# Performance work log

Hardware: AMD Instinct MI355X
Metric: run time of the kernel (lower is better)

## Reference

```python
import jax, jax.numpy as jnp
import numpy as np

EPS = 1e-12  # matches torch F.normalize default eps


def _l2norm(x):
    # F.normalize(x, dim=-1): x / max(||x||, eps)
    n = jnp.sqrt(jnp.sum(x * x, axis=-1, keepdims=True))
    return x / jnp.maximum(n, EPS)


def setup_inputs() -> dict:
    key = jax.random.key(0)
    kq, kk, kv = jax.random.split(key, 3)
    B, H, N, D = 8, 16, 1024, 64
    q = jax.random.normal(kq, (B, H, N, D), dtype=jnp.float32)
    k = jax.random.normal(kk, (B, H, N, D), dtype=jnp.float32)
    v = jax.random.normal(kv, (B, H, N, D), dtype=jnp.float32)
    return {"q": q, "k": k, "v": v}


def reference(q, k, v):
    B, H, N, D = q.shape
    qn = _l2norm(q)  # [B,H,N,D]
    kn = _l2norm(k)  # [B,H,N,D]
    # cosine-similarity attention logits: [B,H,N,N]
    attn = jnp.einsum("bhnd,bhmd->bhnm", qn, kn)
    attn = jax.nn.softmax(attn, axis=-1)
    # attn_drop is identity (p=0)
    x = jnp.einsum("bhnm,bhmd->bhnd", attn, v)  # [B,H,N,D]
    # transpose(1,2).reshape(B, -1, H*D)
    x = jnp.transpose(x, (0, 2, 1, 3)).reshape(B, N, H * D)
    return x
```

## Files before the change

### kernel.cpp

```cpp
#include <hip/hip_runtime.h>
#include <stdint.h>

typedef __attribute__((ext_vector_type(8))) short short8;
typedef __attribute__((ext_vector_type(4))) float floatx4;

#define B_   8
#define H_   16
#define N_   1024
#define D_   64
#define NH_  (B_*H_)
#define LOG2E 1.44269504088896340736f

extern "C" {
__device__ float __ocml_native_exp2_f32(float);
__device__ float __ocml_native_rsqrt_f32(float);
}

__device__ __forceinline__ unsigned int pk2(float a, float b) {
    unsigned int ua = __float_as_uint(a) + 0x8000u;
    unsigned int ub = __float_as_uint(b) + 0x8000u;
    return __builtin_amdgcn_perm(ub, ua, 0x07060302);
}

__global__ __launch_bounds__(256, 2) void attn_fused(
    const float* __restrict__ q, const float* __restrict__ k,
    const float* __restrict__ v, float* __restrict__ out)
{
    __shared__ __align__(16) unsigned short ks[2][64 * 64];
    __shared__ __align__(16) unsigned short vt[2][64 * 64];

    const int bid = blockIdx.x;
    const int xcd = bid & 7, rest = bid >> 3;
    const int qt = rest & 3;
    const int head = (rest >> 2) * 8 + xcd;
    const int tid = threadIdx.x, w = tid >> 6, lane = tid & 63;
    const int lam = lane & 15, quad = lane >> 4;
    const int sw = lam & 7;
    const int q0 = qt * 256 + w * 64;

    const float* qh = q + ((size_t)head * N_ + q0) * D_;
    const float* kh = k + (size_t)head * N_ * D_;
    const float* vh = v + (size_t)head * N_ * D_;

    short8 aq[4][2];
    #pragma unroll
    for (int t = 0; t < 4; t++) {
        const float* qr = qh + (t * 16 + lam) * D_ + quad * 8;
        float4 f0 = *(const float4*)(qr);
        float4 f1 = *(const float4*)(qr + 4);
        float4 f2 = *(const float4*)(qr + 32);
        float4 f3 = *(const float4*)(qr + 36);
        float ss = f0.x*f0.x + f0.y*f0.y + f0.z*f0.z + f0.w*f0.w
                 + f1.x*f1.x + f1.y*f1.y + f1.z*f1.z + f1.w*f1.w
                 + f2.x*f2.x + f2.y*f2.y + f2.z*f2.z + f2.w*f2.w
                 + f3.x*f3.x + f3.y*f3.y + f3.z*f3.z + f3.w*f3.w;
        ss += __shfl_xor(ss, 16);
        ss += __shfl_xor(ss, 32);
        float sc = LOG2E * __ocml_native_rsqrt_f32(ss);
        union { unsigned int u[4]; short8 s8; } p0, p1;
        p0.u[0] = pk2(f0.x*sc, f0.y*sc); p0.u[1] = pk2(f0.z*sc, f0.w*sc);
        p0.u[2] = pk2(f1.x*sc, f1.y*sc); p0.u[3] = pk2(f1.z*sc, f1.w*sc);
        p1.u[0] = pk2(f2.x*sc, f2.y*sc); p1.u[1] = pk2(f2.z*sc, f2.w*sc);
        p1.u[2] = pk2(f3.x*sc, f3.y*sc); p1.u[3] = pk2(f3.z*sc, f3.w*sc);
        aq[t][0] = p0.s8; aq[t][1] = p1.s8;
    }

    floatx4 oacc[4][4];
    #pragma unroll
    for (int t = 0; t < 4; t++)
        #pragma unroll
        for (int dt = 0; dt < 4; dt++) oacc[t][dt] = (floatx4){0.f, 0.f, 0.f, 0.f};
    float l[4] = {0.f, 0.f, 0.f, 0.f};

    const int srow = w * 16 + (lane >> 2);
    const int kd   = (lane & 3) * 8;
    const int ksw  = srow & 7;
    const int vsw  = lane & 7;
    const int cb0  = 2 * w;

    float4 kx[4];
    float  vr[2][8];

    auto gload = [&](int ck) {
        const float* kp = kh + ((size_t)(ck * 64 + srow)) * D_ + kd;
        kx[0] = *(const float4*)(kp);
        kx[1] = *(const float4*)(kp + 4);
        kx[2] = *(const float4*)(kp + 32);
        kx[3] = *(const float4*)(kp + 36);
        #pragma unroll
        for (int cbi = 0; cbi < 2; cbi++) {
            int cb = cb0 + cbi;
            int Lb = ((cb >> 2) << 5) + ((cb & 3) << 2);
            #pragma unroll
            for (int j = 0; j < 8; j++) {
                int L = Lb + ((j >> 2) << 4) + (j & 3);
                vr[cbi][j] = vh[((size_t)(ck * 64 + L)) * D_ + lane];
            }
        }
    };

    auto stage = [&](int buf) {
        float ss = kx[0].x*kx[0].x + kx[0].y*kx[0].y + kx[0].z*kx[0].z + kx[0].w*kx[0].w
                 + kx[1].x*kx[1].x + kx[1].y*kx[1].y + kx[1].z*kx[1].z + kx[1].w*kx[1].w
                 + kx[2].x*kx[2].x + kx[2].y*kx[2].y + kx[2].z*kx[2].z + kx[2].w*kx[2].w
                 + kx[3].x*kx[3].x + kx[3].y*kx[3].y + kx[3].z*kx[3].z + kx[3].w*kx[3].w;
        ss += __shfl_xor(ss, 1);
        ss += __shfl_xor(ss, 2);
        float sc = __ocml_native_rsqrt_f32(ss);
        #pragma unroll
        for (int i = 0; i < 2; i++) {
            float4 a = kx[2 * i], b = kx[2 * i + 1];
            union { unsigned int u[4]; short8 s8; } pk;
            pk.u[0] = pk2(a.x*sc, a.y*sc); pk.u[1] = pk2(a.z*sc, a.w*sc);
            pk.u[2] = pk2(b.x*sc, b.y*sc); pk.u[3] = pk2(b.z*sc, b.w*sc);
            int cbk = (lane & 3) + 4 * i;
            *(short8*)&ks[buf][srow * 64 + ((cbk ^ ksw) << 3)] = pk.s8;
        }
        #pragma unroll
        for (int cbi = 0; cbi < 2; cbi++) {
            union { unsigned int u[4]; short8 s8; } pv;
            pv.u[0] = pk2(vr[cbi][0], vr[cbi][1]); pv.u[1] = pk2(vr[cbi][2], vr[cbi][3]);
            pv.u[2] = pk2(vr[cbi][4], vr[cbi][5]); pv.u[3] = pk2(vr[cbi][6], vr[cbi][7]);
            *(short8*)&vt[buf][lane * 64 + (((cb0 + cbi) ^ vsw) << 3)] = pv.s8;
        }
    };

    auto compute = [&](int buf) {
        const unsigned short* ksb = &ks[buf][0];
        const unsigned short* vsb = &vt[buf][0];
        #pragma unroll
        for (int g = 0; g < 2; g++) {
            floatx4 s[4][2];
            #pragma unroll
            for (int s2 = 0; s2 < 2; s2++) {
                int st = g * 2 + s2;
                short8 bk0 = *(const short8*)(ksb + (st * 16 + lam) * 64 + (((0 + quad) ^ sw) << 3));
                short8 bk1 = *(const short8*)(ksb + (st * 16 + lam) * 64 + (((4 + quad) ^ sw) << 3));
                #pragma unroll
                for (int t = 0; t < 4; t++) {
                    floatx4 acc = (floatx4){0.f, 0.f, 0.f, 0.f};
                    acc = __builtin_amdgcn_mfma_f32_16x16x32_bf16(bk0, aq[t][0], acc, 0, 0, 0);
                    acc = __builtin_amdgcn_mfma_f32_16x16x32_bf16(bk1, aq[t][1], acc, 0, 0, 0);
                    s[t][s2] = acc;
                }
            }
            short8 pa[4];
            #pragma unroll
            for (int t = 0; t < 4; t++) {
                float e00 = __ocml_native_exp2_f32(s[t][0][0]);
                float e01 = __ocml_native_exp2_f32(s[t][0][1]);
                float e02 = __ocml_native_exp2_f32(s[t][0][2]);
                float e03 = __ocml_native_exp2_f32(s[t][0][3]);
                float e10 = __ocml_native_exp2_f32(s[t][1][0]);
                float e11 = __ocml_native_exp2_f32(s[t][1][1]);
                float e12 = __ocml_native_exp2_f32(s[t][1][2]);
                float e13 = __ocml_native_exp2_f32(s[t][1][3]);
                l[t] += ((e00 + e01) + (e02 + e03)) + ((e10 + e11) + (e12 + e13));
                union { unsigned int u[4]; short8 s8; } pk;
                pk.u[0] = pk2(e00, e01); pk.u[1] = pk2(e02, e03);
                pk.u[2] = pk2(e10, e11); pk.u[3] = pk2(e12, e13);
                pa[t] = pk.s8;
            }
            #pragma unroll
            for (int dt = 0; dt < 4; dt++) {
                short8 bv = *(const short8*)(vsb + (dt * 16 + lam) * 64 + (((g * 4 + quad) ^ sw) << 3));
                #pragma unroll
                for (int t = 0; t < 4; t++)
                    oacc[t][dt] = __builtin_amdgcn_mfma_f32_16x16x32_bf16(pa[t], bv, oacc[t][dt], 0, 0, 0);
            }
        }
    };

    gload(0);
    stage(0);
    __syncthreads();
    for (int c = 0; c < 16; ++c) {
        int buf = c & 1;
        if (c < 15) gload(c + 1);
        compute(buf);
        if (c < 15) stage(buf ^ 1);
        __syncthreads();
    }

    const int b = head >> 4, hh = head & 15;
    #pragma unroll
    for (int t = 0; t < 4; t++) {
        float lr = l[t];
        lr += __shfl_xor(lr, 16);
        lr += __shfl_xor(lr, 32);
        float rl = 1.0f / lr;
        float rq[4];
        #pragma unroll
        for (int r = 0; r < 4; r++) rq[r] = __shfl(rl, quad * 4 + r);
        float* ob = out + ((size_t)b * N_ + q0 + t * 16) * (H_ * D_) + hh * 64;
        #pragma unroll
        for (int dt = 0; dt < 4; dt++)
            #pragma unroll
            for (int r = 0; r < 4; r++)
                ob[(quad * 4 + r) * (H_ * D_) + dt * 16 + lam] = oacc[t][dt][r] * rq[r];
    }
}

extern "C" void kernel_launch(void* const* d_in, const int* in_sizes, int n_in,
                              void* d_out, int out_size, void* d_ws, size_t ws_size,
                              hipStream_t stream) {
    const float* q = (const float*)d_in[0];
    const float* k = (const float*)d_in[1];
    const float* v = (const float*)d_in[2];
    float* out = (float*)d_out;
    (void)d_ws; (void)ws_size;
    hipLaunchKernelGGL(attn_fused, dim3(NH_ * 4), dim3(256), 0, stream, q, k, v, out);
}
```

Measured before the change: 164.5 us.

## Split each block's 256 query rows across 8 waves of 32 rows

Doubles the block size from 4 to 8 waves, with each wave now owning 32 query rows instead of 64. The per-thread K/V staging work for each 64-key chunk is halved and the staging index math is rewritten for 8 waves. Each wave holds fewer accumulators, which lowers register pressure and allows more resident waves per CU. The cost is fewer MFMAs per shared-memory K/V fragment read, so LDS read traffic rises relative to compute.

Measured after the change: 159.1 us. -3.3%, faster.

```diff
diff --git a/kernel.cpp b/kernel.cpp
--- a/kernel.cpp
+++ b/kernel.cpp
@@ -22,7 +22,7 @@
     return __builtin_amdgcn_perm(ub, ua, 0x07060302);
 }
 
-__global__ __launch_bounds__(256, 2) void attn_fused(
+__global__ __launch_bounds__(512, 4) void attn_fused(
     const float* __restrict__ q, const float* __restrict__ k,
     const float* __restrict__ v, float* __restrict__ out)
 {
@@ -36,15 +36,15 @@
     const int tid = threadIdx.x, w = tid >> 6, lane = tid & 63;
     const int lam = lane & 15, quad = lane >> 4;
     const int sw = lam & 7;
-    const int q0 = qt * 256 + w * 64;
+    const int q0 = qt * 256 + w * 32;
 
     const float* qh = q + ((size_t)head * N_ + q0) * D_;
     const float* kh = k + (size_t)head * N_ * D_;
     const float* vh = v + (size_t)head * N_ * D_;
 
-    short8 aq[4][2];
+    short8 aq[2][2];
     #pragma unroll
-    for (int t = 0; t < 4; t++) {
+    for (int t = 0; t < 2; t++) {
         const float* qr = qh + (t * 16 + lam) * D_ + quad * 8;
         float4 f0 = *(const float4*)(qr);
         float4 f1 = *(const float4*)(qr + 4);
@@ -65,64 +65,48 @@
         aq[t][0] = p0.s8; aq[t][1] = p1.s8;
     }
 
-    floatx4 oacc[4][4];
+    floatx4 oacc[2][4];
     #pragma unroll
-    for (int t = 0; t < 4; t++)
+    for (int t = 0; t < 2; t++)
         #pragma unroll
         for (int dt = 0; dt < 4; dt++) oacc[t][dt] = (floatx4){0.f, 0.f, 0.f, 0.f};
-    float l[4] = {0.f, 0.f, 0.f, 0.f};
+    float l[2] = {0.f, 0.f};
 
-    const int srow = w * 16 + (lane >> 2);
-    const int kd   = (lane & 3) * 8;
+    const int srow = w * 8 + (lane >> 3);
+    const int cbk  = lane & 7;
     const int ksw  = srow & 7;
-    const int vsw  = lane & 7;
-    const int cb0  = 2 * w;
+    const int Lb   = ((w >> 2) << 5) + ((w & 3) << 2);
+    const int vwin = (w ^ (lane & 7)) << 3;
 
-    float4 kx[4];
-    float  vr[2][8];
+    float4 kx[2];
+    float  vr[8];
 
     auto gload = [&](int ck) {
-        const float* kp = kh + ((size_t)(ck * 64 + srow)) * D_ + kd;
+        const float* kp = kh + ((size_t)(ck * 64 + srow)) * D_ + cbk * 8;
         kx[0] = *(const float4*)(kp);
         kx[1] = *(const float4*)(kp + 4);
-        kx[2] = *(const float4*)(kp + 32);
-        kx[3] = *(const float4*)(kp + 36);
         #pragma unroll
-        for (int cbi = 0; cbi < 2; cbi++) {
-            int cb = cb0 + cbi;
-            int Lb = ((cb >> 2) << 5) + ((cb & 3) << 2);
-            #pragma unroll
-            for (int j = 0; j < 8; j++) {
-                int L = Lb + ((j >> 2) << 4) + (j & 3);
-                vr[cbi][j] = vh[((size_t)(ck * 64 + L)) * D_ + lane];
-            }
+        for (int j = 0; j < 8; j++) {
+            int L = Lb + ((j >> 2) << 4) + (j & 3);
+            vr[j] = vh[((size_t)(ck * 64 + L)) * D_ + lane];
         }
     };
 
     auto stage = [&](int buf) {
         float ss = kx[0].x*kx[0].x + kx[0].y*kx[0].y + kx[0].z*kx[0].z + kx[0].w*kx[0].w
-                 + kx[1].x*kx[1].x + kx[1].y*kx[1].y + kx[1].z*kx[1].z + kx[1].w*kx[1].w
-                 + kx[2].x*kx[2].x + kx[2].y*kx[2].y + kx[2].z*kx[2].z + kx[2].w*kx[2].w
-                 + kx[3].x*kx[3].x + kx[3].y*kx[3].y + kx[3].z*kx[3].z + kx[3].w*kx[3].w;
+                 + kx[1].x*kx[1].x + kx[1].y*kx[1].y + kx[1].z*kx[1].z + kx[1].w*kx[1].w;
         ss += __shfl_xor(ss, 1);
         ss += __shfl_xor(ss, 2);
+        ss += __shfl_xor(ss, 4);
         float sc = __ocml_native_rsqrt_f32(ss);
-        #pragma unroll
-        for (int i = 0; i < 2; i++) {
-            float4 a = kx[2 * i], b = kx[2 * i + 1];
-            union { unsigned int u[4]; short8 s8; } pk;
-            pk.u[0] = pk2(a.x*sc, a.y*sc); pk.u[1] = pk2(a.z*sc, a.w*sc);
-            pk.u[2] = pk2(b.x*sc, b.y*sc); pk.u[3] = pk2(b.z*sc, b.w*sc);
-            int cbk = (lane & 3) + 4 * i;
-            *(short8*)&ks[buf][srow * 64 + ((cbk ^ ksw) << 3)] = pk.s8;
-        }
-        #pragma unroll
-        for (int cbi = 0; cbi < 2; cbi++) {
-            union { unsigned int u[4]; short8 s8; } pv;
-            pv.u[0] = pk2(vr[cbi][0], vr[cbi][1]); pv.u[1] = pk2(vr[cbi][2], vr[cbi][3]);
-            pv.u[2] = pk2(vr[cbi][4], vr[cbi][5]); pv.u[3] = pk2(vr[cbi][6], vr[cbi][7]);
-            *(short8*)&vt[buf][lane * 64 + (((cb0 + cbi) ^ vsw) << 3)] = pv.s8;
-        }
+        union { unsigned int u[4]; short8 s8; } pk;
+        pk.u[0] = pk2(kx[0].x*sc, kx[0].y*sc); pk.u[1] = pk2(kx[0].z*sc, kx[0].w*sc);
+        pk.u[2] = pk2(kx[1].x*sc, kx[1].y*sc); pk.u[3] = pk2(kx[1].z*sc, kx[1].w*sc);
+        *(short8*)&ks[buf][srow * 64 + ((cbk ^ ksw) << 3)] = pk.s8;
+        union { unsigned int u[4]; short8 s8; } pv;
+        pv.u[0] = pk2(vr[0], vr[1]); pv.u[1] = pk2(vr[2], vr[3]);
+        pv.u[2] = pk2(vr[4], vr[5]); pv.u[3] = pk2(vr[6], vr[7]);
+        *(short8*)&vt[buf][lane * 64 + vwin] = pv.s8;
     };
 
     auto compute = [&](int buf) {
@@ -130,23 +114,23 @@
         const unsigned short* vsb = &vt[buf][0];
         #pragma unroll
         for (int g = 0; g < 2; g++) {
-            floatx4 s[4][2];
+            floatx4 s[2][2];
             #pragma unroll
             for (int s2 = 0; s2 < 2; s2++) {
                 int st = g * 2 + s2;
                 short8 bk0 = *(const short8*)(ksb + (st * 16 + lam) * 64 + (((0 + quad) ^ sw) << 3));
                 short8 bk1 = *(const short8*)(ksb + (st * 16 + lam) * 64 + (((4 + quad) ^ sw) << 3));
                 #pragma unroll
-                for (int t = 0; t < 4; t++) {
+                for (int t = 0; t < 2; t++) {
                     floatx4 acc = (floatx4){0.f, 0.f, 0.f, 0.f};
                     acc = __builtin_amdgcn_mfma_f32_16x16x32_bf16(bk0, aq[t][0], acc, 0, 0, 0);
                     acc = __builtin_amdgcn_mfma_f32_16x16x32_bf16(bk1, aq[t][1], acc, 0, 0, 0);
                     s[t][s2] = acc;
                 }
             }
-            short8 pa[4];
+            short8 pa[2];
             #pragma unroll
-            for (int t = 0; t < 4; t++) {
+            for (int t = 0; t < 2; t++) {
                 float e00 = __ocml_native_exp2_f32(s[t][0][0]);
                 float e01 = __ocml_native_exp2_f32(s[t][0][1]);
                 float e02 = __ocml_native_exp2_f32(s[t][0][2]);
@@ -165,7 +149,7 @@
             for (int dt = 0; dt < 4; dt++) {
                 short8 bv = *(const short8*)(vsb + (dt * 16 + lam) * 64 + (((g * 4 + quad) ^ sw) << 3));
                 #pragma unroll
-                for (int t = 0; t < 4; t++)
+                for (int t = 0; t < 2; t++)
                     oacc[t][dt] = __builtin_amdgcn_mfma_f32_16x16x32_bf16(pa[t], bv, oacc[t][dt], 0, 0, 0);
             }
         }
@@ -184,7 +168,7 @@
 
     const int b = head >> 4, hh = head & 15;
     #pragma unroll
-    for (int t = 0; t < 4; t++) {
+    for (int t = 0; t < 2; t++) {
         float lr = l[t];
         lr += __shfl_xor(lr, 16);
         lr += __shfl_xor(lr, 32);
@@ -209,5 +193,5 @@
     const float* v = (const float*)d_in[2];
     float* out = (float*)d_out;
     (void)d_ws; (void)ws_size;
-    hipLaunchKernelGGL(attn_fused, dim3(NH_ * 4), dim3(256), 0, stream, q, k, v, out);
+    hipLaunchKernelGGL(attn_fused, dim3(NH_ * 4), dim3(512), 0, stream, q, k, v, out);
 }
```
